# Kernel tuning notes

Hardware: AMD Instinct MI355X
Metric: run time of the kernel (lower is better)

Reference implementation:

```python
import jax, jax.numpy as jnp
import numpy as np

THRESHOLD = 0.3

def setup_inputs() -> dict:
    key = jax.random.key(0)
    ks = jax.random.split(key, 8)
    B, T, N, d = 4, 32, 1024, 2
    hd, od, hs, osz = 64, 64, 128, 2
    p = lambda k, sh: jax.random.normal(k, sh, jnp.float32) * 0.1
    return {
        "points": jax.random.uniform(ks[0], (B, T, N, d), jnp.float32),
        "W1": p(ks[1], (hd, d)),   "b1": jnp.zeros((hd,), jnp.float32),
        "W2": p(ks[2], (od, hd)),  "b2": jnp.zeros((od,), jnp.float32),
        "Wg": p(ks[3], (hd, od)),  "bg": jnp.zeros((hd,), jnp.float32),
        "Wih": p(ks[4], (3 * hs, hd)), "Whh": p(ks[5], (3 * hs, hs)),
        "bih": jnp.zeros((3 * hs,), jnp.float32), "bhh": jnp.zeros((3 * hs,), jnp.float32),
        "Wf": p(ks[6], (osz, hs)), "bf": jnp.zeros((osz,), jnp.float32),
    }

def _gcn_step(pts, W1, b1, W2, b2, Wg, bg):
    # pts: [N, d]. Torch detaches node features & adjacency (no grad to points).
    pts = jax.lax.stop_gradient(pts)
    dist = jnp.linalg.norm(pts[:, None, :] - pts[None, :, :], axis=2)  # [N,N]
    A = (dist < THRESHOLD).astype(pts.dtype)
    dinv = 1.0 / jnp.sqrt(A.sum(axis=1))          # rowsum >= 1 (self-loop)
    An = A * dinv[:, None] * dinv[None, :]        # D^{-1/2} A D^{-1/2}
    x = jax.nn.relu((An @ pts) @ W1.T + b1)       # [N, hd]
    x = jax.nn.relu((An @ x) @ W2.T + b2)         # [N, od]
    return x.mean(axis=0) @ Wg.T + bg             # [hd]

def reference(points, W1, b1, W2, b2, Wg, bg, Wih, Whh, bih, bhh, Wf, bf):
    # GCN per (batch, time): [B, T, hd]
    gcn = jax.vmap(jax.vmap(lambda p: _gcn_step(p, W1, b1, W2, b2, Wg, bg)))(points)
    H = Whh.shape[1]

    def gru_step(h, x):  # torch GRU gate order: r, z, n
        gi = x @ Wih.T + bih
        gh = h @ Whh.T + bhh
        ir, iz, inn = jnp.split(gi, 3)
        hr, hz, hn = jnp.split(gh, 3)
        r = jax.nn.sigmoid(ir + hr)
        z = jax.nn.sigmoid(iz + hz)
        n = jnp.tanh(inn + r * hn)
        h_new = (1.0 - z) * n + z * h
        return h_new, h_new

    h0 = jnp.zeros((H,), points.dtype)
    run = lambda xs: jax.lax.scan(gru_step, h0, xs)[1]   # [T, H]
    hs = jax.vmap(run)(gcn)                              # [B, T, H]
    y = hs @ Wf.T + bf                                   # [B, T, out]
    # torch: per-element gru_out.mean(dim=1, keepdim=True) on [1,T,out] -> [1,1,out], stacked -> [B,1,1,out]
    return y.mean(axis=1, keepdims=True)[:, :, None, :]
```

## Files before the change

### kernel.cpp

```cpp
#include <hip/hip_runtime.h>
#include <hip/hip_bf16.h>
#include <math.h>

#define N_PTS 1024
#define BT    128
typedef unsigned int u32;
typedef __attribute__((ext_vector_type(8))) short short8_t;
typedef __attribute__((ext_vector_type(4))) float f32x4;

__device__ __forceinline__ float bfi(u32 bits16) {
    union { u32 u; float f; } v; v.u = bits16 << 16; return v.f;
}
__device__ __forceinline__ unsigned short f2bf(float f) {
    union { float f; u32 u; } v; v.f = f;
    return (unsigned short)((v.u + 0x7FFFu + ((v.u >> 16) & 1u)) >> 16);
}
__device__ __forceinline__ float ldf(const void* p, int i, bool bf) {
    return bf ? bfi(((const unsigned short*)p)[i]) : ((const float*)p)[i];
}
__device__ __forceinline__ float2 ldp(const void* pbase, int j, bool bf) {
    if (bf) {
        u32 w = ((const u32*)pbase)[j];
        return make_float2(bfi(w & 0xFFFFu), bfi(w >> 16));
    }
    return ((const float2*)pbase)[j];
}
__device__ __forceinline__ bool detect_bf16(const void* pts, int tid, int* s_flag) {
    if (tid < 64) {
        u32 w = ((const u32*)pts)[tid];
        float v = bfi(w & 0xFFFFu);
        bool ok = (v >= 0.0f) && (v <= 1.0f);
        unsigned long long m = __ballot(ok);
        if (tid == 0) *s_flag = (m == 0xFFFFFFFFFFFFFFFFull) ? 1 : 0;
    }
    __syncthreads();
    return *s_flag != 0;
}
__device__ __forceinline__ bool is_nb(float px, float py, float qx, float qy) {
    float dx = px - qx, dy = py - qy;
    float d2 = __fadd_rn(__fmul_rn(dx, dx), __fmul_rn(dy, dy));
    return d2 < 0.09f;
}
__device__ __forceinline__ const void* pts_base(const void* pts, int bt, bool bf) {
    return bf ? (const void*)((const unsigned short*)pts + (size_t)bt * N_PTS * 2)
              : (const void*)((const float*)pts + (size_t)bt * N_PTS * 2);
}
__device__ __forceinline__ void gload16(const u32* g, u32* l) {
    __builtin_amdgcn_global_load_lds((const __attribute__((address_space(1))) u32*)g,
                                     (__attribute__((address_space(3))) u32*)l, 16, 0, 0);
}
__device__ __forceinline__ float rdlane(float v, int i) {
    return __int_as_float(__builtin_amdgcn_readlane(__float_as_int(v), i));
}

__global__ __launch_bounds__(256) void k1_bm(const void* __restrict__ pts,
                                             float* __restrict__ dinv,
                                             float* __restrict__ gsum,
                                             u32* __restrict__ bm) {
    int blk = blockIdx.x, tid = threadIdx.x;
    int bt = blk >> 2, q = blk & 3;
    __shared__ float2 sp[N_PTS];
    __shared__ int s_flag;
    bool bf = detect_bf16(pts, tid, &s_flag);
    const void* pb = pts_base(pts, bt, bf);
    for (int j = tid; j < N_PTS; j += 256) sp[j] = ldp(pb, j, bf);
    if (blk < 32) gsum[blk * 256 + tid] = 0.0f;
    __syncthreads();
    int i = q * 256 + tid;
    float px = sp[i].x, py = sp[i].y;
    const float4* sp4 = (const float4*)sp;
    u32* bmrow = bm + (size_t)bt * 32768 + i;
    int cnt = 0;
    for (int c = 0; c < 32; c++) {
        u32 m = 0;
#pragma unroll
        for (int h = 0; h < 8; h++) {
            float4 s01 = sp4[c * 16 + 2 * h], s23 = sp4[c * 16 + 2 * h + 1];
            if (is_nb(px, py, s01.x, s01.y)) m |= 1u << (4 * h);
            if (is_nb(px, py, s01.z, s01.w)) m |= 1u << (4 * h + 1);
            if (is_nb(px, py, s23.x, s23.y)) m |= 1u << (4 * h + 2);
            if (is_nb(px, py, s23.z, s23.w)) m |= 1u << (4 * h + 3);
        }
        bmrow[c * 1024] = m;
        cnt += __popc(m);
    }
    dinv[bt * N_PTS + i] = 1.0f / sqrtf((float)cnt);
}

__global__ __launch_bounds__(256) void k2_x1v(const void* __restrict__ pts,
                                              const void* __restrict__ W1,
                                              const void* __restrict__ b1,
                                              const float* __restrict__ dinv,
                                              const u32* __restrict__ bm,
                                              u32* __restrict__ x1vB) {
    int blk = blockIdx.x, tid = threadIdx.x;
    int bt = blk >> 2, q = blk & 3;
    __shared__ float2 sud[N_PTS];
    __shared__ float2 sax[256];
    __shared__ float  sdl[256];
    __shared__ int s_flag;
    bool bf = detect_bf16(pts, tid, &s_flag);
    const void* pb = pts_base(pts, bt, bf);
    for (int j = tid; j < N_PTS; j += 256) {
        float2 p = ldp(pb, j, bf);
        float d = dinv[bt * N_PTS + j];
        sud[j] = make_float2(d * p.x, d * p.y);
    }
    __syncthreads();
    int i = q * 256 + tid;
    float ax = 0.f, ay = 0.f;
    const u32* bmr = bm + (size_t)bt * 32768 + i;
    for (int c = 0; c < 32; c++) {
        u32 m = bmr[c * 1024];
        const float4* uv = (const float4*)sud + c * 16;
#pragma unroll
        for (int h = 0; h < 16; h++) {
            float4 v = uv[h];
            bool b0 = (m >> (2 * h)) & 1u, b1_ = (m >> (2 * h + 1)) & 1u;
            ax += b0 ? v.x : 0.0f;  ay += b0 ? v.y : 0.0f;
            ax += b1_ ? v.z : 0.0f; ay += b1_ ? v.w : 0.0f;
        }
    }
    float di = dinv[bt * N_PTS + i];
    sax[tid] = make_float2(ax * di, ay * di);
    sdl[tid] = di;
    __syncthreads();
    int ch = tid & 63, wq = tid >> 6;
    float w0 = ldf(W1, 2 * ch, bf), w1v = ldf(W1, 2 * ch + 1, bf), bb = ldf(b1, ch, bf);
    for (int tt = 0; tt < 4; tt++) {
        u32 ow[8];
#pragma unroll
        for (int k2i = 0; k2i < 8; k2i++) {
            int lj = tt * 64 + wq * 16 + 2 * k2i;
            float2 a0 = sax[lj], a1 = sax[lj + 1];
            float v0 = sdl[lj]     * fmaxf(fmaf(w0, a0.x, fmaf(w1v, a0.y, bb)), 0.0f);
            float v1 = sdl[lj + 1] * fmaxf(fmaf(w0, a1.x, fmaf(w1v, a1.y, bb)), 0.0f);
            ow[k2i] = (u32)f2bf(v0) | ((u32)f2bf(v1) << 16);
        }
        u32* dst = x1vB + ((size_t)(bt * 16 + q * 4 + tt) * 64 + ch) * 36 + wq * 8;
        *(uint4*)dst = make_uint4(ow[0], ow[1], ow[2], ow[3]);
        *(uint4*)(dst + 4) = make_uint4(ow[4], ow[5], ow[6], ow[7]);
    }
}

__global__ __launch_bounds__(256) void k3_mfma(const void* __restrict__ pts,
                                               const void* __restrict__ W2,
                                               const void* __restrict__ b2,
                                               const float* __restrict__ dinv,
                                               const u32* __restrict__ bm,
                                               const u32* __restrict__ x1vB,
                                               float* __restrict__ gsum) {
    __shared__ u32 pool[15424];
    __shared__ int s_flag;
    float* poolf = (float*)pool;
    int tid = threadIdx.x, lane = tid & 63, w = tid >> 6;
    int l15 = lane & 15, quad = lane >> 4;
    int blk = blockIdx.x, bt = blk & 127, rowblk = blk >> 7;
    bool bf = detect_bf16(pts, tid, &s_flag);

    const u32* xg = x1vB + (size_t)bt * 36864;
    for (int it = w; it < 9; it += 4)
        gload16(xg + it * 256 + lane * 4, pool + 8192 + it * 256 + lane * 4);

    const u32* bg_ = bm + (size_t)bt * 32768 + rowblk * 256;
    for (int idx = tid; idx < 8192; idx += 256) {
        int c = idx >> 8, r = idx & 255;
        pool[idx] = bg_[c * 1024 + r];
    }
    unsigned short* W2B = (unsigned short*)(pool + 12800);
    for (int idx = tid; idx < 4096; idx += 256) {
        int o = idx >> 6, c = idx & 63;
        W2B[o * 72 + c] = f2bf(ldf(W2, idx, bf));
    }
    if (tid < 256) poolf[15104 + tid] = dinv[bt * N_PTS + rowblk * 256 + tid];
    if (tid < 64)  poolf[15360 + tid] = ldf(b2, tid, bf);

    f32x4 acc[4][4];
#pragma unroll
    for (int rf = 0; rf < 4; rf++)
#pragma unroll
        for (int nb = 0; nb < 4; nb++)
#pragma unroll
            for (int r = 0; r < 4; r++) acc[rf][nb][r] = 0.0f;

    for (int t = 0; t < 16; t++) {
        __syncthreads();
        if (t + 1 < 16) {
            u32* dst = pool + ((t & 1) ? 8192 : 10496);
            const u32* src = xg + (t + 1) * 2304;
            for (int it = w; it < 9; it += 4)
                gload16(src + it * 256 + lane * 4, dst + it * 256 + lane * 4);
        }
        const unsigned short* xf = (const unsigned short*)(pool + ((t & 1) ? 10496 : 8192));
#pragma unroll
        for (int ks = 0; ks < 2; ks++) {
            short8_t bq[4];
#pragma unroll
            for (int rf = 0; rf < 4; rf++) {
                u32 mw = pool[(2 * t + ks) * 256 + w * 64 + rf * 16 + l15];
                u32 by = (mw >> (quad * 8)) & 0xFFu;
                short8_t v;
#pragma unroll
                for (int i2 = 0; i2 < 8; i2++)
                    v[i2] = (by & (1u << i2)) ? (short)0x3F80 : (short)0;
                bq[rf] = v;
            }
#pragma unroll
            for (int nb = 0; nb < 4; nb++) {
                short8_t af = *(const short8_t*)(xf + (nb * 16 + l15) * 72 + ks * 32 + quad * 8);
#pragma unroll
                for (int rf = 0; rf < 4; rf++)
                    acc[rf][nb] = __builtin_amdgcn_mfma_f32_16x16x32_bf16(af, bq[rf], acc[rf][nb], 0, 0, 0);
            }
        }
    }
    __syncthreads();

    u32* dump = pool;
#pragma unroll
    for (int rf = 0; rf < 4; rf++) {
        int rn = w * 64 + rf * 16 + l15;
        float di = poolf[15104 + rn];
#pragma unroll
        for (int nb = 0; nb < 4; nb++) {
            u32 lo = (u32)f2bf(acc[rf][nb][0] * di) | ((u32)f2bf(acc[rf][nb][1] * di) << 16);
            u32 hi = (u32)f2bf(acc[rf][nb][2] * di) | ((u32)f2bf(acc[rf][nb][3] * di) << 16);
            u32* dst = dump + rn * 36 + nb * 8 + quad * 2;
            dst[0] = lo; dst[1] = hi;
        }
    }
    __syncthreads();
    f32x4 xacc[4][4];
#pragma unroll
    for (int ob = 0; ob < 4; ob++)
#pragma unroll
        for (int rf = 0; rf < 4; rf++)
#pragma unroll
            for (int r = 0; r < 4; r++) xacc[ob][rf][r] = 0.0f;
#pragma unroll
    for (int ks2 = 0; ks2 < 2; ks2++) {
        short8_t b2f[4];
#pragma unroll
        for (int rf = 0; rf < 4; rf++)
            b2f[rf] = *(const short8_t*)((const unsigned short*)dump +
                        (w * 64 + rf * 16 + l15) * 72 + ks2 * 32 + quad * 8);
#pragma unroll
        for (int ob = 0; ob < 4; ob++) {
            short8_t a2 = *(const short8_t*)(W2B + (ob * 16 + l15) * 72 + ks2 * 32 + quad * 8);
#pragma unroll
            for (int rf = 0; rf < 4; rf++)
                xacc[ob][rf] = __builtin_amdgcn_mfma_f32_16x16x32_bf16(a2, b2f[rf], xacc[ob][rf], 0, 0, 0);
        }
    }
#pragma unroll
    for (int ob = 0; ob < 4; ob++) {
#pragma unroll
        for (int r = 0; r < 4; r++) {
            int o = ob * 16 + quad * 4 + r;
            float bb = poolf[15360 + o];
            float s = 0.0f;
#pragma unroll
            for (int rf = 0; rf < 4; rf++) s += fmaxf(xacc[ob][rf][r] + bb, 0.0f);
            s += __shfl_down(s, 8, 16);
            s += __shfl_down(s, 4, 16);
            s += __shfl_down(s, 2, 16);
            s += __shfl_down(s, 1, 16);
            if (l15 == 0) atomicAdd(&gsum[bt * 64 + o], s);
        }
    }
}

__global__ __launch_bounds__(768, 1) void k4_all(const void* __restrict__ pts,
                                                 const void* __restrict__ Wg,
                                                 const void* __restrict__ bg,
                                                 const void* __restrict__ Wih,
                                                 const void* __restrict__ Whh,
                                                 const void* __restrict__ bih,
                                                 const void* __restrict__ bhh,
                                                 const void* __restrict__ Wf,
                                                 const void* __restrict__ bf_,
                                                 const float* __restrict__ gsum,
                                                 float* __restrict__ out) {
    int b = blockIdx.x, tid = threadIdx.x;
    __shared__ float s_gi[32 * 384];
    __shared__ float sWgT[64 * 65];
    __shared__ float s_gm[2048];
    __shared__ float s_x[2048];
    __shared__ float s_part[768];
    __shared__ float s_h[128];
    __shared__ int s_flag;
    bool bf = detect_bf16(pts, tid, &s_flag);
    for (int idx = tid; idx < 4096; idx += 768) {
        int o = idx >> 6, k = idx & 63;
        sWgT[k * 65 + o] = ldf(Wg, idx, bf);
    }
    for (int idx = tid; idx < 2048; idx += 768)
        s_gm[idx] = gsum[(size_t)b * 2048 + idx] * (1.0f / 1024.0f);
    if (tid < 128) s_h[tid] = 0.0f;
    __syncthreads();
    for (int idx = tid; idx < 2048; idx += 768) {
        int t = idx >> 6, c = idx & 63;
        float s0 = ldf(bg, c, bf), s1 = 0.f, s2 = 0.f, s3 = 0.f;
        const float* gm = s_gm + t * 64;
#pragma unroll
        for (int k = 0; k < 64; k += 4) {
            s0 = fmaf(sWgT[k * 65 + c],       gm[k],     s0);
            s1 = fmaf(sWgT[(k + 1) * 65 + c], gm[k + 1], s1);
            s2 = fmaf(sWgT[(k + 2) * 65 + c], gm[k + 2], s2);
            s3 = fmaf(sWgT[(k + 3) * 65 + c], gm[k + 3], s3);
        }
        s_x[idx] = (s0 + s1) + (s2 + s3);
    }
    __syncthreads();
    int hi = (tid >= 384) ? 1 : 0;
    int r = tid - hi * 384;
    int lane = tid & 63;
    {
        float wv[64];
        if (bf) {
#pragma unroll
            for (int k = 0; k < 64; k++) wv[k] = bfi(((const unsigned short*)Wih)[r * 64 + k]);
        } else {
            const float4* wr = (const float4*)Wih + r * 16;
#pragma unroll
            for (int qq = 0; qq < 16; qq++) {
                float4 v = wr[qq];
                wv[4*qq] = v.x; wv[4*qq+1] = v.y; wv[4*qq+2] = v.z; wv[4*qq+3] = v.w;
            }
        }
        float br = ldf(bih, r, bf);
        for (int t = hi; t < 32; t += 2) {
            float xv = s_x[t * 64 + lane];
            float s0 = br, s1 = 0.f, s2 = 0.f, s3 = 0.f;
#pragma unroll
            for (int k = 0; k < 64; k += 4) {
                s0 = fmaf(wv[k],     rdlane(xv, k),     s0);
                s1 = fmaf(wv[k + 1], rdlane(xv, k + 1), s1);
                s2 = fmaf(wv[k + 2], rdlane(xv, k + 2), s2);
                s3 = fmaf(wv[k + 3], rdlane(xv, k + 3), s3);
            }
            s_gi[t * 384 + r] = (s0 + s1) + (s2 + s3);
        }
    }
    float wh2[64];
    {
        int koff = hi * 64;
        if (bf) {
#pragma unroll
            for (int k = 0; k < 64; k++)
                wh2[k] = bfi(((const unsigned short*)Whh)[r * 128 + koff + k]);
        } else {
            const float4* wr = (const float4*)Whh + (r * 128 + koff) / 4;
#pragma unroll
            for (int qq = 0; qq < 16; qq++) {
                float4 v = wr[qq];
                wh2[4*qq] = v.x; wh2[4*qq+1] = v.y; wh2[4*qq+2] = v.z; wh2[4*qq+3] = v.w;
            }
        }
    }
    float bhr = hi ? 0.0f : ldf(bhh, r, bf);
    float h_reg = 0.0f, hsum = 0.0f;
    __syncthreads();

    for (int t = 0; t < 32; t++) {
        float hval = s_h[hi * 64 + lane];
        float s0 = bhr, s1 = 0.f, s2 = 0.f, s3 = 0.f;
#pragma unroll
        for (int k = 0; k < 64; k += 4) {
            s0 = fmaf(wh2[k],     rdlane(hval, k),     s0);
            s1 = fmaf(wh2[k + 1], rdlane(hval, k + 1), s1);
            s2 = fmaf(wh2[k + 2], rdlane(hval, k + 2), s2);
            s3 = fmaf(wh2[k + 3], rdlane(hval, k + 3), s3);
        }
        s_part[tid] = (s0 + s1) + (s2 + s3);
        __syncthreads();
        if (tid < 128) {
            int c = tid;
            float gr = s_gi[t * 384 + c]       + s_part[c]       + s_part[384 + c];
            float gz = s_gi[t * 384 + 128 + c] + s_part[128 + c] + s_part[512 + c];
            float gn = s_gi[t * 384 + 256 + c];
            float hn = s_part[256 + c] + s_part[640 + c];
            float rr = 1.0f / (1.0f + expf(-gr));
            float z  = 1.0f / (1.0f + expf(-gz));
            float n  = tanhf(fmaf(rr, hn, gn));
            float hnew = (1.0f - z) * n + z * h_reg;
            h_reg = hnew; hsum += hnew; s_h[c] = hnew;
        }
        __syncthreads();
    }
    if (tid < 128) {
        float hm = hsum * (1.0f / 32.0f);
        s_part[tid]       = ldf(Wf, tid, bf) * hm;
        s_part[128 + tid] = ldf(Wf, 128 + tid, bf) * hm;
    }
    __syncthreads();
    if (tid < 2) {
        float s = ldf(bf_, tid, bf);
        for (int k = 0; k < 128; k++) s += s_part[tid * 128 + k];
        out[b * 2 + tid] = s;
    }
}

extern "C" void kernel_launch(void* const* d_in, const int* in_sizes, int n_in,
                              void* d_out, int out_size, void* d_ws, size_t ws_size,
                              hipStream_t stream) {
    const void* pts = d_in[0];
    const void* W1  = d_in[1];
    const void* b1  = d_in[2];
    const void* W2  = d_in[3];
    const void* b2  = d_in[4];
    const void* Wg  = d_in[5];
    const void* bg  = d_in[6];
    const void* Wih = d_in[7];
    const void* Whh = d_in[8];
    const void* bih = d_in[9];
    const void* bhh = d_in[10];
    const void* Wf  = d_in[11];
    const void* bf_ = d_in[12];

    float* dinv = (float*)d_ws;
    float* gsum = dinv + (size_t)BT * N_PTS;
    u32*   bm   = (u32*)(gsum + BT * 64);
    u32*   x1vB = bm + (size_t)BT * 32768;

    k1_bm  <<<512, 256, 0, stream>>>(pts, dinv, gsum, bm);
    k2_x1v <<<512, 256, 0, stream>>>(pts, W1, b1, dinv, bm, x1vB);
    k3_mfma<<<512, 256, 0, stream>>>(pts, W2, b2, dinv, bm, x1vB, gsum);
    k4_all <<<4, 768, 0, stream>>>(pts, Wg, bg, Wih, Whh, bih, bhh, Wf, bf_,
                                   gsum, (float*)d_out);
}
```

Measured before the change: 238.5 us.

## Compute first GCN layer via bf16 MFMA and parallelize GRU gate update

The first aggregation layer is rewritten so the bitmask adjacency times the dinv-scaled point features, pre-multiplied by W1, runs as bf16 MFMA. Previously each thread did a per-bit select loop over all 1024 neighbours. The bitmask tile is staged transposed in LDS, and outputs are staged through LDS for coalesced stores. The GRU loop now has every thread redundantly compute the gate update, with double-buffered partials, which removes one barrier per step and the idle threads. It also uses fast exp and divide approximations for sigmoid and tanh, and the W1 projection is now applied before aggregation in bf16, which adds rounding error.

```diff
diff --git a/kernel.cpp b/kernel.cpp
--- a/kernel.cpp
+++ b/kernel.cpp
@@ -14,6 +14,11 @@
 __device__ __forceinline__ unsigned short f2bf(float f) {
     union { float f; u32 u; } v; v.f = f;
     return (unsigned short)((v.u + 0x7FFFu + ((v.u >> 16) & 1u)) >> 16);
+}
+__device__ __forceinline__ u32 pkbf(float a, float b) {
+    union { __hip_bfloat162 b2; u32 u; } cv;
+    cv.b2 = __float22bfloat162_rn(make_float2(a, b));
+    return cv.u;
 }
 __device__ __forceinline__ float ldf(const void* p, int i, bool bf) {
     return bf ? bfi(((const unsigned short*)p)[i]) : ((const float*)p)[i];
@@ -51,6 +56,12 @@
 }
 __device__ __forceinline__ float rdlane(float v, int i) {
     return __int_as_float(__builtin_amdgcn_readlane(__float_as_int(v), i));
+}
+__device__ __forceinline__ float sigm(float x) {
+    return __fdividef(1.0f, 1.0f + __expf(-x));
+}
+__device__ __forceinline__ float tanh_f(float x) {
+    return fmaf(2.0f, __fdividef(1.0f, 1.0f + __expf(-2.0f * x)), -1.0f);
 }
 
 __global__ __launch_bounds__(256) void k1_bm(const void* __restrict__ pts,
@@ -87,18 +98,24 @@
     dinv[bt * N_PTS + i] = 1.0f / sqrtf((float)cnt);
 }
 
-__global__ __launch_bounds__(256) void k2_x1v(const void* __restrict__ pts,
-                                              const void* __restrict__ W1,
-                                              const void* __restrict__ b1,
-                                              const float* __restrict__ dinv,
-                                              const u32* __restrict__ bm,
-                                              u32* __restrict__ x1vB) {
-    int blk = blockIdx.x, tid = threadIdx.x;
-    int bt = blk >> 2, q = blk & 3;
-    __shared__ float2 sud[N_PTS];
-    __shared__ float2 sax[256];
-    __shared__ float  sdl[256];
+__global__ __launch_bounds__(256) void k3a_x1v(const void* __restrict__ pts,
+                                               const void* __restrict__ W1,
+                                               const void* __restrict__ b1,
+                                               const float* __restrict__ dinv,
+                                               const u32* __restrict__ bm,
+                                               u32* __restrict__ x1vB) {
+    __shared__ u32 pool[10944];
     __shared__ int s_flag;
+    float* poolf = (float*)pool;
+    float2* sud = (float2*)pool;
+    u32* bmL = pool + 2048;
+    float* sdiL = poolf + 10496;
+    float* b1L = poolf + 10752;
+    float* W1L = poolf + 10816;
+    int tid = threadIdx.x, lane = tid & 63, w = tid >> 6;
+    int l15 = lane & 15, quad = lane >> 4;
+    int blk = blockIdx.x, bt = blk & 127, rowblk = blk >> 7;
+    int rowbase = rowblk * 256;
     bool bf = detect_bf16(pts, tid, &s_flag);
     const void* pb = pts_base(pts, bt, bf);
     for (int j = tid; j < N_PTS; j += 256) {
@@ -106,40 +123,87 @@
         float d = dinv[bt * N_PTS + j];
         sud[j] = make_float2(d * p.x, d * p.y);
     }
-    __syncthreads();
-    int i = q * 256 + tid;
-    float ax = 0.f, ay = 0.f;
-    const u32* bmr = bm + (size_t)bt * 32768 + i;
-    for (int c = 0; c < 32; c++) {
-        u32 m = bmr[c * 1024];
-        const float4* uv = (const float4*)sud + c * 16;
-#pragma unroll
-        for (int h = 0; h < 16; h++) {
-            float4 v = uv[h];
-            bool b0 = (m >> (2 * h)) & 1u, b1_ = (m >> (2 * h + 1)) & 1u;
-            ax += b0 ? v.x : 0.0f;  ay += b0 ? v.y : 0.0f;
-            ax += b1_ ? v.z : 0.0f; ay += b1_ ? v.w : 0.0f;
-        }
-    }
-    float di = dinv[bt * N_PTS + i];
-    sax[tid] = make_float2(ax * di, ay * di);
-    sdl[tid] = di;
-    __syncthreads();
-    int ch = tid & 63, wq = tid >> 6;
-    float w0 = ldf(W1, 2 * ch, bf), w1v = ldf(W1, 2 * ch + 1, bf), bb = ldf(b1, ch, bf);
-    for (int tt = 0; tt < 4; tt++) {
-        u32 ow[8];
-#pragma unroll
-        for (int k2i = 0; k2i < 8; k2i++) {
-            int lj = tt * 64 + wq * 16 + 2 * k2i;
-            float2 a0 = sax[lj], a1 = sax[lj + 1];
-            float v0 = sdl[lj]     * fmaxf(fmaf(w0, a0.x, fmaf(w1v, a0.y, bb)), 0.0f);
-            float v1 = sdl[lj + 1] * fmaxf(fmaf(w0, a1.x, fmaf(w1v, a1.y, bb)), 0.0f);
-            ow[k2i] = (u32)f2bf(v0) | ((u32)f2bf(v1) << 16);
-        }
-        u32* dst = x1vB + ((size_t)(bt * 16 + q * 4 + tt) * 64 + ch) * 36 + wq * 8;
-        *(uint4*)dst = make_uint4(ow[0], ow[1], ow[2], ow[3]);
-        *(uint4*)(dst + 4) = make_uint4(ow[4], ow[5], ow[6], ow[7]);
+    sdiL[tid] = dinv[bt * N_PTS + rowbase + tid];
+    for (int idx = tid; idx < 8192; idx += 256) {
+        int c = idx >> 8, r = idx & 255;
+        bmL[r * 33 + c] = bm[(size_t)bt * 32768 + c * 1024 + rowbase + r];
+    }
+    if (tid < 128) W1L[tid] = ldf(W1, tid, bf);
+    if (tid < 64)  b1L[tid] = ldf(b1, tid, bf);
+    __syncthreads();
+
+    float w0v[4], w1v[4], b1v[4];
+#pragma unroll
+    for (int nb = 0; nb < 4; nb++) {
+        int ch = nb * 16 + l15;
+        w0v[nb] = W1L[2 * ch]; w1v[nb] = W1L[2 * ch + 1]; b1v[nb] = b1L[ch];
+    }
+    f32x4 acc[4][4];
+#pragma unroll
+    for (int rf = 0; rf < 4; rf++)
+#pragma unroll
+        for (int nb = 0; nb < 4; nb++)
+#pragma unroll
+            for (int r = 0; r < 4; r++) acc[rf][nb][r] = 0.0f;
+
+    for (int ks = 0; ks < 32; ks++) {
+        const float4* u4 = (const float4*)(sud + ks * 32 + quad * 8);
+        float4 U0 = u4[0], U1 = u4[1], U2 = u4[2], U3 = u4[3];
+        float pxd[8] = {U0.x, U0.z, U1.x, U1.z, U2.x, U2.z, U3.x, U3.z};
+        float pyd[8] = {U0.y, U0.w, U1.y, U1.w, U2.y, U2.w, U3.y, U3.w};
+        short8_t bz[4];
+#pragma unroll
+        for (int nb = 0; nb < 4; nb++) {
+            union { short8_t v; u32 d[4]; } cv;
+#pragma unroll
+            for (int p = 0; p < 4; p++) {
+                float z0 = fmaf(pxd[2 * p],     w0v[nb], pyd[2 * p]     * w1v[nb]);
+                float z1 = fmaf(pxd[2 * p + 1], w0v[nb], pyd[2 * p + 1] * w1v[nb]);
+                cv.d[p] = pkbf(z0, z1);
+            }
+            bz[nb] = cv.v;
+        }
+#pragma unroll
+        for (int rf = 0; rf < 4; rf++) {
+            u32 word = bmL[(w * 64 + rf * 16 + l15) * 33 + ks];
+            u32 by = (word >> (quad * 8)) & 0xFFu;
+            short8_t av;
+#pragma unroll
+            for (int i2 = 0; i2 < 8; i2++)
+                av[i2] = (by & (1u << i2)) ? (short)0x3F80 : (short)0;
+#pragma unroll
+            for (int nb = 0; nb < 4; nb++)
+                acc[rf][nb] = __builtin_amdgcn_mfma_f32_16x16x32_bf16(av, bz[nb], acc[rf][nb], 0, 0, 0);
+        }
+    }
+    __syncthreads();
+    u32* dumpX = pool + 2048;
+#pragma unroll
+    for (int rf = 0; rf < 4; rf++) {
+        float4 dv = *(const float4*)(sdiL + w * 64 + rf * 16 + quad * 4);
+        float dva[4] = {dv.x, dv.y, dv.z, dv.w};
+#pragma unroll
+        for (int nb = 0; nb < 4; nb++) {
+            int ch = nb * 16 + l15;
+            float xo[4];
+#pragma unroll
+            for (int r = 0; r < 4; r++) {
+                float tq = fmaf(dva[r], acc[rf][nb][r], b1v[nb]);
+                xo[r] = dva[r] * fmaxf(tq, 0.0f);
+            }
+            u32 dbase = (u32)(ch * 132 + w * 32 + rf * 8 + quad * 2);
+            *(uint2*)(dumpX + dbase) = make_uint2(pkbf(xo[0], xo[1]), pkbf(xo[2], xo[3]));
+        }
+    }
+    __syncthreads();
+    int ch = tid >> 2, seg = tid & 3;
+    u32* gbase = x1vB + ((size_t)(bt * 16 + rowblk * 4) * 64) * 36;
+#pragma unroll
+    for (int t4 = 0; t4 < 4; t4++) {
+        const uint4* src = (const uint4*)(dumpX + ch * 132 + t4 * 32 + seg * 8);
+        uint4 v0 = src[0], v1 = src[1];
+        u32* dst = gbase + ((size_t)(t4 * 64 + ch)) * 36 + seg * 8;
+        *(uint4*)dst = v0; *(uint4*)(dst + 4) = v1;
     }
 }
 
@@ -282,12 +346,13 @@
                                                  const float* __restrict__ gsum,
                                                  float* __restrict__ out) {
     int b = blockIdx.x, tid = threadIdx.x;
-    __shared__ float s_gi[32 * 384];
+    __shared__ float s_gir[4096];
+    __shared__ float s_giz[4096];
+    __shared__ float s_gin[4096];
     __shared__ float sWgT[64 * 65];
     __shared__ float s_gm[2048];
     __shared__ float s_x[2048];
-    __shared__ float s_part[768];
-    __shared__ float s_h[128];
+    __shared__ float s_pt[2 * 6 * 128];
     __shared__ int s_flag;
     bool bf = detect_bf16(pts, tid, &s_flag);
     for (int idx = tid; idx < 4096; idx += 768) {
@@ -296,7 +361,6 @@
     }
     for (int idx = tid; idx < 2048; idx += 768)
         s_gm[idx] = gsum[(size_t)b * 2048 + idx] * (1.0f / 1024.0f);
-    if (tid < 128) s_h[tid] = 0.0f;
     __syncthreads();
     for (int idx = tid; idx < 2048; idx += 768) {
         int t = idx >> 6, c = idx & 63;
@@ -314,18 +378,22 @@
     __syncthreads();
     int hi = (tid >= 384) ? 1 : 0;
     int r = tid - hi * 384;
+    int g = r >> 7;
+    int cpart = r & 127;
     int lane = tid & 63;
+    int wv = tid >> 6;
+    float* gdst = (g == 0) ? s_gir : (g == 1) ? s_giz : s_gin;
     {
-        float wv[64];
+        float wvr[64];
         if (bf) {
 #pragma unroll
-            for (int k = 0; k < 64; k++) wv[k] = bfi(((const unsigned short*)Wih)[r * 64 + k]);
+            for (int k = 0; k < 64; k++) wvr[k] = bfi(((const unsigned short*)Wih)[r * 64 + k]);
         } else {
             const float4* wr = (const float4*)Wih + r * 16;
 #pragma unroll
             for (int qq = 0; qq < 16; qq++) {
                 float4 v = wr[qq];
-                wv[4*qq] = v.x; wv[4*qq+1] = v.y; wv[4*qq+2] = v.z; wv[4*qq+3] = v.w;
+                wvr[4*qq] = v.x; wvr[4*qq+1] = v.y; wvr[4*qq+2] = v.z; wvr[4*qq+3] = v.w;
             }
         }
         float br = ldf(bih, r, bf);
@@ -334,12 +402,12 @@
             float s0 = br, s1 = 0.f, s2 = 0.f, s3 = 0.f;
 #pragma unroll
             for (int k = 0; k < 64; k += 4) {
-                s0 = fmaf(wv[k],     rdlane(xv, k),     s0);
-                s1 = fmaf(wv[k + 1], rdlane(xv, k + 1), s1);
-                s2 = fmaf(wv[k + 2], rdlane(xv, k + 2), s2);
-                s3 = fmaf(wv[k + 3], rdlane(xv, k + 3), s3);
-            }
-            s_gi[t * 384 + r] = (s0 + s1) + (s2 + s3);
+                s0 = fmaf(wvr[k],     rdlane(xv, k),     s0);
+                s1 = fmaf(wvr[k + 1], rdlane(xv, k + 1), s1);
+                s2 = fmaf(wvr[k + 2], rdlane(xv, k + 2), s2);
+                s3 = fmaf(wvr[k + 3], rdlane(xv, k + 3), s3);
+            }
+            gdst[t * 128 + cpart] = (s0 + s1) + (s2 + s3);
         }
     }
     float wh2[64];
@@ -359,44 +427,46 @@
         }
     }
     float bhr = hi ? 0.0f : ldf(bhh, r, bf);
-    float h_reg = 0.0f, hsum = 0.0f;
+    int slot = g * 2 + hi;
+    int cg = hi * 64 + lane;
+    float h_self = 0.0f, hsum = 0.0f;
     __syncthreads();
 
     for (int t = 0; t < 32; t++) {
-        float hval = s_h[hi * 64 + lane];
         float s0 = bhr, s1 = 0.f, s2 = 0.f, s3 = 0.f;
 #pragma unroll
         for (int k = 0; k < 64; k += 4) {
-            s0 = fmaf(wh2[k],     rdlane(hval, k),     s0);
-            s1 = fmaf(wh2[k + 1], rdlane(hval, k + 1), s1);
-            s2 = fmaf(wh2[k + 2], rdlane(hval, k + 2), s2);
-            s3 = fmaf(wh2[k + 3], rdlane(hval, k + 3), s3);
-        }
-        s_part[tid] = (s0 + s1) + (s2 + s3);
+            s0 = fmaf(wh2[k],     rdlane(h_self, k),     s0);
+            s1 = fmaf(wh2[k + 1], rdlane(h_self, k + 1), s1);
+            s2 = fmaf(wh2[k + 2], rdlane(h_self, k + 2), s2);
+            s3 = fmaf(wh2[k + 3], rdlane(h_self, k + 3), s3);
+        }
+        float* buf = s_pt + (t & 1) * 768;
+        buf[slot * 128 + cpart] = (s0 + s1) + (s2 + s3);
         __syncthreads();
-        if (tid < 128) {
-            int c = tid;
-            float gr = s_gi[t * 384 + c]       + s_part[c]       + s_part[384 + c];
-            float gz = s_gi[t * 384 + 128 + c] + s_part[128 + c] + s_part[512 + c];
-            float gn = s_gi[t * 384 + 256 + c];
-            float hn = s_part[256 + c] + s_part[640 + c];
-            float rr = 1.0f / (1.0f + expf(-gr));
-            float z  = 1.0f / (1.0f + expf(-gz));
-            float n  = tanhf(fmaf(rr, hn, gn));
-            float hnew = (1.0f - z) * n + z * h_reg;
-            h_reg = hnew; hsum += hnew; s_h[c] = hnew;
-        }
-        __syncthreads();
-    }
+        float gr = s_gir[t * 128 + cg] + buf[0 * 128 + cg] + buf[1 * 128 + cg];
+        float gz = s_giz[t * 128 + cg] + buf[2 * 128 + cg] + buf[3 * 128 + cg];
+        float hn = buf[4 * 128 + cg] + buf[5 * 128 + cg];
+        float rr = sigm(gr);
+        float zz = sigm(gz);
+        float gn = fmaf(rr, hn, s_gin[t * 128 + cg]);
+        float n  = tanh_f(gn);
+        float hnew = fmaf(zz, h_self - n, n);
+        h_self = hnew; hsum += hnew;
+    }
+    float* sfin = s_gm;
+    if (wv == 0) sfin[lane] = hsum;
+    if (wv == 6) sfin[64 + lane] = hsum;
+    __syncthreads();
     if (tid < 128) {
-        float hm = hsum * (1.0f / 32.0f);
-        s_part[tid]       = ldf(Wf, tid, bf) * hm;
-        s_part[128 + tid] = ldf(Wf, 128 + tid, bf) * hm;
+        float hm = sfin[tid] * (1.0f / 32.0f);
+        sfin[256 + tid] = ldf(Wf, tid, bf) * hm;
+        sfin[384 + tid] = ldf(Wf, 128 + tid, bf) * hm;
     }
     __syncthreads();
     if (tid < 2) {
         float s = ldf(bf_, tid, bf);
-        for (int k = 0; k < 128; k++) s += s_part[tid * 128 + k];
+        for (int k = 0; k < 128; k++) s += sfin[256 + tid * 128 + k];
         out[b * 2 + tid] = s;
     }
 }
@@ -424,7 +494,7 @@
     u32*   x1vB = bm + (size_t)BT * 32768;
 
     k1_bm  <<<512, 256, 0, stream>>>(pts, dinv, gsum, bm);
-    k2_x1v <<<512, 256, 0, stream>>>(pts, W1, b1, dinv, bm, x1vB);
+    k3a_x1v<<<512, 256, 0, stream>>>(pts, W1, b1, dinv, bm, x1vB);
     k3_mfma<<<512, 256, 0, stream>>>(pts, W2, b2, dinv, bm, x1vB, gsum);
     k4_all <<<4, 768, 0, stream>>>(pts, Wg, bg, Wih, Whh, bih, bhh, Wf, bf_,
                                    gsum, (float*)d_out);
```

Measured after the change: 241.1 us. No clear change (+1.1%).
